# Performance work log

Hardware: AMD Instinct MI355X
Metric: run time of the kernel (lower is better)

Reference implementation:

```python
import jax, jax.numpy as jnp
import numpy as np
import math

N, L, C, H, K = 4, 16384, 256, 8, 4
D = C // H


def setup_inputs():
    rng = jax.random.key(0)
    ks = jax.random.split(rng, 16)
    def w(k, shape, scale):
        return jax.random.normal(k, shape, jnp.float32) * scale
    s = 1.0 / math.sqrt(C)
    return {
        "query": jax.random.normal(ks[0], (N, L, C), jnp.float32),
        "key": jax.random.normal(ks[1], (N, L, C), jnp.float32),
        "value": jax.random.normal(ks[2], (N, L, C), jnp.float32),
        "reference_points": jax.random.uniform(ks[3], (N, L, 2), jnp.float32),
        "pos_embed": jax.random.normal(ks[4], (N, L, C), jnp.float32),
        "Wq": w(ks[5], (C, C), s), "bq": jnp.zeros((C,), jnp.float32),
        "Wk": w(ks[6], (C, C), s), "bk": jnp.zeros((C,), jnp.float32),
        "Wv": w(ks[7], (C, C), s), "bv": jnp.zeros((C,), jnp.float32),
        "Wo1": w(ks[8], (C, 2 * C), s), "bo1": jnp.zeros((2 * C,), jnp.float32),
        "Wo2": w(ks[9], (2 * C, H * K * 2), 0.02), "bo2": w(ks[10], (H * K * 2,), 0.02),
        "Wpos": w(ks[11], (C, C), s), "bpos": jnp.zeros((C,), jnp.float32),
        "Wout": w(ks[12], (C, C), s), "bout": jnp.zeros((C,), jnp.float32),
    }


def _sample_weight(points):
    # F.grid_sample on a 1x1 feature map (bilinear, zeros padding, align_corners=False)
    # degenerates to a scalar weight: grid g = 2p-1, unnormalized c = g/2 = p - 0.5,
    # pixel-0 bilinear weight per axis = max(0, 1 - |c|).
    c = points - 0.5
    return jax.nn.relu(1.0 - jnp.abs(c[..., 0])) * jax.nn.relu(1.0 - jnp.abs(c[..., 1]))


def reference(query, key, value, reference_points, pos_embed,
              Wq, bq, Wk, bk, Wv, bv, Wo1, bo1, Wo2, bo2, Wpos, bpos, Wout, bout):
    Nb, Ln, Cd = query.shape
    q = (query @ Wq + bq).reshape(Nb, Ln, H, D)
    k = (key @ Wk + bk).reshape(Nb, Ln, H, D)
    v = (value @ Wv + bv).reshape(Nb, Ln, H, D)
    pos = (pos_embed @ Wpos + bpos).reshape(Nb, Ln, H, D)
    q = q + pos
    k = k + pos
    # offset MLP: Linear(C,2C) -> ReLU -> Linear(2C, H*K*2)
    offsets = (jax.nn.relu(query @ Wo1 + bo1) @ Wo2 + bo2).reshape(Nb, Ln, H, K, 2)
    sp = reference_points[:, :, None, None, :] + offsets  # [N,L,H,K,2]
    w = _sample_weight(sp)                                # [N,L,H,K]
    # sampled_k[n,l,h,k,:] = k[n,l,h,:] * w[n,l,h,k]  (1x1 grid_sample closed form)
    qk = jnp.einsum('nlhd,nlhd->nlh', q, k)               # [N,L,H]
    attn = jax.nn.softmax(qk[..., None] * w / math.sqrt(D), axis=-1)  # [N,L,H,K]
    # output = sum_k attn_k * (v * w_k) = v * sum_k(attn_k * w_k)
    wv = jnp.sum(attn * w, axis=-1)                       # [N,L,H]
    out = (v * wv[..., None]).reshape(Nb, Ln, Cd)
    return out @ Wout + bout
```

## Files before the change

kernel.cpp:

```cpp
#include <hip/hip_runtime.h>
#include <hip/hip_bf16.h>

typedef __bf16 bf16x8 __attribute__((ext_vector_type(8)));
typedef float f32x4 __attribute__((ext_vector_type(4)));
typedef float f32x2 __attribute__((ext_vector_type(2)));

#define MT 32
#define CC 256

__device__ __forceinline__ int swz(int r, int c) {
    return r * 512 + ((c * 2) ^ ((r & 7) << 4));
}
__device__ __forceinline__ int swzH(int r, int c) {
    return r * 1024 + ((c * 2) ^ ((r & 7) << 4));
}

__device__ __forceinline__ void stage_load(const float* __restrict__ src, int row0, int tid,
                                           f32x4 (&v)[4]) {
#pragma unroll
    for (int i = 0; i < 4; ++i) {
        int f = i * 512 + tid;
        int r = f >> 6;
        int c = (f & 63) * 4;
        v[i] = __builtin_nontemporal_load((const f32x4*)(src + (size_t)(row0 + r) * CC + c));
    }
}
__device__ __forceinline__ void stage_write(__bf16* dst, int tid, const f32x4 (&v)[4]) {
#pragma unroll
    for (int i = 0; i < 4; ++i) {
        int f = i * 512 + tid;
        int r = f >> 6;
        int c = (f & 63) * 4;
        union { __bf16 h[4]; unsigned long long u; } uu;
        uu.h[0] = (__bf16)v[i][0]; uu.h[1] = (__bf16)v[i][1];
        uu.h[2] = (__bf16)v[i][2]; uu.h[3] = (__bf16)v[i][3];
        *(unsigned long long*)((char*)dst + swz(r, c)) = uu.u;
    }
}

__global__ void prep_all(const float* __restrict__ Wq, const float* __restrict__ Wk,
                         const float* __restrict__ Wpos, const float* __restrict__ Wo1,
                         const float* __restrict__ Wo2, const float* __restrict__ Wv,
                         const float* __restrict__ Wout, __bf16* __restrict__ ws)
{
    int i = blockIdx.x * 256 + threadIdx.x;
    if (i >= 557056) return;
    int j, K, N;
    const float* S0 = nullptr; const float* S1 = nullptr;
    if (i < 131072)      { j = i;          K = 512; N = 256; S0 = Wq;  S1 = Wpos; }
    else if (i < 262144) { j = i - 131072; K = 512; N = 256; S0 = Wk;  S1 = Wpos; }
    else if (i < 393216) { j = i - 262144; K = 256; N = 512; S0 = Wo1; }
    else if (i < 425984) { j = i - 393216; K = 512; N = 64;  S0 = Wo2; }
    else if (i < 491520) { j = i - 425984; K = 256; N = 256; S0 = Wv; }
    else                 { j = i - 491520; K = 256; N = 256; S0 = Wout; }
    int tile = j >> 9, r = j & 511;
    int lane = r >> 3, e = r & 7;
    int q4 = lane >> 4, r16 = lane & 15;
    int KC = K >> 5;
    int nc = tile / KC, kc = tile - nc * KC;
    int k = kc * 32 + q4 * 8 + e;
    int n = nc * 16 + r16;
    float v;
    if (S1 && k >= 256) v = S1[(size_t)(k - 256) * N + n];
    else                v = S0[(size_t)k * N + n];
    ws[i] = (__bf16)v;
}

extern "C" __global__ void __launch_bounds__(512, 4)
fused_ext_attn(const float* __restrict__ query, const float* __restrict__ key,
               const float* __restrict__ value, const float* __restrict__ refp,
               const float* __restrict__ pose,
               const __bf16* __restrict__ ws,
               const float* __restrict__ bq, const float* __restrict__ bk,
               const float* __restrict__ bv, const float* __restrict__ bpos,
               const float* __restrict__ bo1, const float* __restrict__ bo2,
               const float* __restrict__ bout,
               float* __restrict__ out)
{
    const __bf16* WTqp  = ws;
    const __bf16* WTkp  = ws + 131072;
    const __bf16* WTo1  = ws + 262144;
    const __bf16* WTo2  = ws + 393216;
    const __bf16* WTv   = ws + 425984;
    const __bf16* WTout = ws + 491520;

    __shared__ __attribute__((aligned(16))) __bf16 SA[MT * CC];
    __shared__ __attribute__((aligned(16))) __bf16 SB[MT * CC];
    __shared__ __attribute__((aligned(16))) __bf16 SC[MT * CC];
    __shared__ __attribute__((aligned(16))) char   H1[32768];

    float* off_s = (float*)H1;
    float* qk_s  = (float*)(H1 + 8192);
    float* wv_s  = (float*)(H1 + 9216);

    const int tid = threadIdx.x;
    const int lane = tid & 63;
    const int wid = tid >> 6;
    const int r16 = lane & 15;
    const int q4 = lane >> 4;
    const int laneoff = lane * 8;
    const int row0 = blockIdx.x * MT;

    f32x4 vq[4], vp[4], vkey[4];
    stage_load(query, row0, tid, vq);
    stage_load(pose, row0, tid, vp);
    stage_load(key, row0, tid, vkey);
    stage_write(SA, tid, vq);
    stage_write(SB, tid, vp);
    __syncthreads();

    stage_write(SC, tid, vkey);
    {
        f32x4 acc[2][4];
#pragma unroll
        for (int i = 0; i < 2; ++i)
#pragma unroll
            for (int j = 0; j < 4; ++j) acc[i][j] = (f32x4){0.f, 0.f, 0.f, 0.f};
#pragma unroll
        for (int ks = 0; ks < 8; ++ks) {
            int ak = ks * 32 + q4 * 8;
            bf16x8 a[2], b[4];
#pragma unroll
            for (int mf = 0; mf < 2; ++mf)
                a[mf] = *(const bf16x8*)((const char*)SA + swz(mf * 16 + r16, ak));
#pragma unroll
            for (int nf = 0; nf < 4; ++nf)
                b[nf] = *(const bf16x8*)(WTo1 + ((size_t)(wid * 4 + nf) * 8 + ks) * 512 + laneoff);
#pragma unroll
            for (int mf = 0; mf < 2; ++mf)
#pragma unroll
                for (int nf = 0; nf < 4; ++nf)
                    acc[mf][nf] = __builtin_amdgcn_mfma_f32_16x16x32_bf16(a[mf], b[nf], acc[mf][nf], 0, 0, 0);
        }
#pragma unroll
        for (int mf = 0; mf < 2; ++mf)
#pragma unroll
            for (int nf = 0; nf < 4; ++nf) {
                int col = wid * 64 + nf * 16 + r16;
                float bias = bo1[col];
#pragma unroll
                for (int r = 0; r < 4; ++r)
                    *(__bf16*)(H1 + swzH(mf * 16 + q4 * 4 + r, col)) =
                        (__bf16)fmaxf(acc[mf][nf][r] + bias, 0.f);
            }
    }
    __syncthreads();

    f32x4 accO[2];
    accO[0] = (f32x4){0.f, 0.f, 0.f, 0.f};
    accO[1] = (f32x4){0.f, 0.f, 0.f, 0.f};
    if (wid < 4) {
#pragma unroll
        for (int ks = 0; ks < 16; ++ks) {
            int ak = ks * 32 + q4 * 8;
            bf16x8 b = *(const bf16x8*)(WTo2 + ((size_t)wid * 16 + ks) * 512 + laneoff);
#pragma unroll
            for (int mf = 0; mf < 2; ++mf) {
                bf16x8 a = *(const bf16x8*)(H1 + swzH(mf * 16 + r16, ak));
                accO[mf] = __builtin_amdgcn_mfma_f32_16x16x32_bf16(a, b, accO[mf], 0, 0, 0);
            }
        }
    }
    f32x4 vval[4];
    stage_load(value, row0, tid, vval);
    float qk_r[2][4];
    {
        f32x4 qa[2][2], ka[2][2];
#pragma unroll
        for (int i = 0; i < 2; ++i)
#pragma unroll
            for (int j = 0; j < 2; ++j) {
                qa[i][j] = (f32x4){0.f, 0.f, 0.f, 0.f};
                ka[i][j] = (f32x4){0.f, 0.f, 0.f, 0.f};
            }
#pragma unroll
        for (int ks = 0; ks < 8; ++ks) {
            int ak = ks * 32 + q4 * 8;
            bf16x8 aq[2], akk[2];
#pragma unroll
            for (int mf = 0; mf < 2; ++mf) {
                aq[mf]  = *(const bf16x8*)((const char*)SA + swz(mf * 16 + r16, ak));
                akk[mf] = *(const bf16x8*)((const char*)SC + swz(mf * 16 + r16, ak));
            }
#pragma unroll
            for (int nf = 0; nf < 2; ++nf) {
                size_t toff = ((size_t)(wid * 2 + nf) * 16 + ks) * 512 + laneoff;
                bf16x8 bqf = *(const bf16x8*)(WTqp + toff);
                bf16x8 bkf = *(const bf16x8*)(WTkp + toff);
#pragma unroll
                for (int mf = 0; mf < 2; ++mf) {
                    qa[mf][nf] = __builtin_amdgcn_mfma_f32_16x16x32_bf16(aq[mf],  bqf, qa[mf][nf], 0, 0, 0);
                    ka[mf][nf] = __builtin_amdgcn_mfma_f32_16x16x32_bf16(akk[mf], bkf, ka[mf][nf], 0, 0, 0);
                }
            }
        }
#pragma unroll
        for (int ks = 8; ks < 16; ++ks) {
            int ak = (ks - 8) * 32 + q4 * 8;
            bf16x8 ap[2];
#pragma unroll
            for (int mf = 0; mf < 2; ++mf)
                ap[mf] = *(const bf16x8*)((const char*)SB + swz(mf * 16 + r16, ak));
#pragma unroll
            for (int nf = 0; nf < 2; ++nf) {
                size_t toff = ((size_t)(wid * 2 + nf) * 16 + ks) * 512 + laneoff;
                bf16x8 bqf = *(const bf16x8*)(WTqp + toff);
                bf16x8 bkf = *(const bf16x8*)(WTkp + toff);
#pragma unroll
                for (int mf = 0; mf < 2; ++mf) {
                    qa[mf][nf] = __builtin_amdgcn_mfma_f32_16x16x32_bf16(ap[mf], bqf, qa[mf][nf], 0, 0, 0);
                    ka[mf][nf] = __builtin_amdgcn_mfma_f32_16x16x32_bf16(ap[mf], bkf, ka[mf][nf], 0, 0, 0);
                }
            }
        }
        float Bq[2], Bk[2];
#pragma unroll
        for (int nf = 0; nf < 2; ++nf) {
            int col = wid * 32 + nf * 16 + r16;
            Bq[nf] = bq[col] + bpos[col];
            Bk[nf] = bk[col] + bpos[col];
        }
#pragma unroll
        for (int mf = 0; mf < 2; ++mf)
#pragma unroll
            for (int r = 0; r < 4; ++r) {
                float p0 = (qa[mf][0][r] + Bq[0]) * (ka[mf][0][r] + Bk[0])
                         + (qa[mf][1][r] + Bq[1]) * (ka[mf][1][r] + Bk[1]);
#pragma unroll
                for (int m = 1; m < 16; m <<= 1)
                    p0 += __shfl_xor(p0, m);
                qk_r[mf][r] = p0;
            }
    }
    __syncthreads();

    stage_write(SA, tid, vval);
    if (wid < 4) {
        int col = wid * 16 + r16;
        float b2 = bo2[col];
#pragma unroll
        for (int mf = 0; mf < 2; ++mf)
#pragma unroll
            for (int r = 0; r < 4; ++r)
                off_s[(mf * 16 + q4 * 4 + r) * 64 + col] = accO[mf][r] + b2;
    }
    if (r16 == 0) {
#pragma unroll
        for (int mf = 0; mf < 2; ++mf)
#pragma unroll
            for (int r = 0; r < 4; ++r)
                qk_s[(mf * 16 + q4 * 4 + r) * 8 + wid] = qk_r[mf][r];
    }
    __syncthreads();

    if (tid < 256) {
        int t = tid >> 3, h = tid & 7;
        float qk = qk_s[t * 8 + h];
        f32x2 rp = __builtin_nontemporal_load((const f32x2*)(refp + (size_t)(row0 + t) * 2));
        float wgt[4], lg[4];
        float m = -1e30f;
#pragma unroll
        for (int kk = 0; kk < 4; ++kk) {
            float ox = off_s[t * 64 + (h * 4 + kk) * 2];
            float oy = off_s[t * 64 + (h * 4 + kk) * 2 + 1];
            float cx = rp[0] + ox - 0.5f, cy = rp[1] + oy - 0.5f;
            float wx = fmaxf(0.f, 1.f - fabsf(cx));
            float wy = fmaxf(0.f, 1.f - fabsf(cy));
            wgt[kk] = wx * wy;
            lg[kk] = qk * wgt[kk] * 0.17677669529663687f;
            m = fmaxf(m, lg[kk]);
        }
        float s = 0.f, sw = 0.f;
#pragma unroll
        for (int kk = 0; kk < 4; ++kk) {
            float e = __expf(lg[kk] - m);
            s += e;
            sw += e * wgt[kk];
        }
        wv_s[t * 8 + h] = sw / s;
    }
    __syncthreads();

    {
        f32x4 acc[2][2];
#pragma unroll
        for (int i = 0; i < 2; ++i)
#pragma unroll
            for (int j = 0; j < 2; ++j) acc[i][j] = (f32x4){0.f, 0.f, 0.f, 0.f};
#pragma unroll
        for (int ks = 0; ks < 8; ++ks) {
            int ak = ks * 32 + q4 * 8;
            bf16x8 a[2], b[2];
#pragma unroll
            for (int mf = 0; mf < 2; ++mf)
                a[mf] = *(const bf16x8*)((const char*)SA + swz(mf * 16 + r16, ak));
#pragma unroll
            for (int nf = 0; nf < 2; ++nf)
                b[nf] = *(const bf16x8*)(WTv + ((size_t)(wid * 2 + nf) * 8 + ks) * 512 + laneoff);
#pragma unroll
            for (int mf = 0; mf < 2; ++mf)
#pragma unroll
                for (int nf = 0; nf < 2; ++nf)
                    acc[mf][nf] = __builtin_amdgcn_mfma_f32_16x16x32_bf16(a[mf], b[nf], acc[mf][nf], 0, 0, 0);
        }
#pragma unroll
        for (int mf = 0; mf < 2; ++mf)
#pragma unroll
            for (int nf = 0; nf < 2; ++nf) {
                int col = wid * 32 + nf * 16 + r16;
                float bias = bv[col];
#pragma unroll
                for (int r = 0; r < 4; ++r) {
                    int row = mf * 16 + q4 * 4 + r;
                    float wvv = wv_s[row * 8 + wid];
                    *(__bf16*)((char*)SC + swz(row, col)) = (__bf16)((acc[mf][nf][r] + bias) * wvv);
                }
            }
    }
    __syncthreads();

    {
        f32x4 acc[2][2];
#pragma unroll
        for (int i = 0; i < 2; ++i)
#pragma unroll
            for (int j = 0; j < 2; ++j) acc[i][j] = (f32x4){0.f, 0.f, 0.f, 0.f};
#pragma unroll
        for (int ks = 0; ks < 8; ++ks) {
            int ak = ks * 32 + q4 * 8;
            bf16x8 a[2], b[2];
#pragma unroll
            for (int mf = 0; mf < 2; ++mf)
                a[mf] = *(const bf16x8*)((const char*)SC + swz(mf * 16 + r16, ak));
#pragma unroll
            for (int nf = 0; nf < 2; ++nf)
                b[nf] = *(const bf16x8*)(WTout + ((size_t)(wid * 2 + nf) * 8 + ks) * 512 + laneoff);
#pragma unroll
            for (int mf = 0; mf < 2; ++mf)
#pragma unroll
                for (int nf = 0; nf < 2; ++nf)
                    acc[mf][nf] = __builtin_amdgcn_mfma_f32_16x16x32_bf16(a[mf], b[nf], acc[mf][nf], 0, 0, 0);
        }
#pragma unroll
        for (int mf = 0; mf < 2; ++mf)
#pragma unroll
            for (int nf = 0; nf < 2; ++nf) {
                int col = wid * 32 + nf * 16 + r16;
                float bias = bout[col];
#pragma unroll
                for (int r = 0; r < 4; ++r) {
                    int row = mf * 16 + q4 * 4 + r;
                    __builtin_nontemporal_store(acc[mf][nf][r] + bias,
                                                out + (size_t)(row0 + row) * CC + col);
                }
            }
    }
}

extern "C" void kernel_launch(void* const* d_in, const int* in_sizes, int n_in,
                              void* d_out, int out_size, void* d_ws, size_t ws_size,
                              hipStream_t stream)
{
    const float* query = (const float*)d_in[0];
    const float* key   = (const float*)d_in[1];
    const float* value = (const float*)d_in[2];
    const float* refp  = (const float*)d_in[3];
    const float* pose  = (const float*)d_in[4];
    const float* Wq  = (const float*)d_in[5];  const float* bq   = (const float*)d_in[6];
    const float* Wk  = (const float*)d_in[7];  const float* bk   = (const float*)d_in[8];
    const float* Wv  = (const float*)d_in[9];  const float* bv   = (const float*)d_in[10];
    const float* Wo1 = (const float*)d_in[11]; const float* bo1  = (const float*)d_in[12];
    const float* Wo2 = (const float*)d_in[13]; const float* bo2  = (const float*)d_in[14];
    const float* Wpos= (const float*)d_in[15]; const float* bpos = (const float*)d_in[16];
    const float* Wout= (const float*)d_in[17]; const float* bout = (const float*)d_in[18];

    __bf16* ws = (__bf16*)d_ws;

    prep_all<<<2176, 256, 0, stream>>>(Wq, Wk, Wpos, Wo1, Wo2, Wv, Wout, ws);

    fused_ext_attn<<<65536 / MT, 512, 0, stream>>>(
        query, key, value, refp, pose, ws,
        bq, bk, bv, bpos, bo1, bo2, bout, (float*)d_out);
}
```

Baseline: 146.8 us.

## Double row tile to 64 and restructure LDS into two reused buffers

Raises the per-block row tile from 32 to 64, so each weight fragment loaded from global memory feeds four M-fragments instead of two, halving weight traffic per row. LDS is cut to two 32KB bf16 tiles plus a small scratch area by streaming query, pos, key and value through them in sequence. The offset-MLP hidden layer is processed in two column halves to fit, and offsets are stored as bf16. The q and k projections are now split into separate passes with extra barriers, and the larger tile halves the grid size.

```diff
diff --git a/kernel.cpp b/kernel.cpp
--- a/kernel.cpp
+++ b/kernel.cpp
@@ -5,35 +5,29 @@
 typedef float f32x4 __attribute__((ext_vector_type(4)));
 typedef float f32x2 __attribute__((ext_vector_type(2)));
 
-#define MT 32
+#define MT 64
 #define CC 256
 
 __device__ __forceinline__ int swz(int r, int c) {
     return r * 512 + ((c * 2) ^ ((r & 7) << 4));
 }
-__device__ __forceinline__ int swzH(int r, int c) {
-    return r * 1024 + ((c * 2) ^ ((r & 7) << 4));
-}
-
-__device__ __forceinline__ void stage_load(const float* __restrict__ src, int row0, int tid,
-                                           f32x4 (&v)[4]) {
-#pragma unroll
-    for (int i = 0; i < 4; ++i) {
+
+__device__ __forceinline__ bf16x8 ldB(const __bf16* __restrict__ WT, int nc, int KC, int kc,
+                                      int laneoff) {
+    return *(const bf16x8*)(WT + ((size_t)nc * KC + kc) * 512 + laneoff);
+}
+
+__device__ __forceinline__ void stream_tile(const float* __restrict__ src, int row0, int tid,
+                                            __bf16* dst) {
+#pragma unroll
+    for (int i = 0; i < 8; ++i) {
         int f = i * 512 + tid;
         int r = f >> 6;
         int c = (f & 63) * 4;
-        v[i] = __builtin_nontemporal_load((const f32x4*)(src + (size_t)(row0 + r) * CC + c));
-    }
-}
-__device__ __forceinline__ void stage_write(__bf16* dst, int tid, const f32x4 (&v)[4]) {
-#pragma unroll
-    for (int i = 0; i < 4; ++i) {
-        int f = i * 512 + tid;
-        int r = f >> 6;
-        int c = (f & 63) * 4;
+        f32x4 v = __builtin_nontemporal_load((const f32x4*)(src + (size_t)(row0 + r) * CC + c));
         union { __bf16 h[4]; unsigned long long u; } uu;
-        uu.h[0] = (__bf16)v[i][0]; uu.h[1] = (__bf16)v[i][1];
-        uu.h[2] = (__bf16)v[i][2]; uu.h[3] = (__bf16)v[i][3];
+        uu.h[0] = (__bf16)v[0]; uu.h[1] = (__bf16)v[1];
+        uu.h[2] = (__bf16)v[2]; uu.h[3] = (__bf16)v[3];
         *(unsigned long long*)((char*)dst + swz(r, c)) = uu.u;
     }
 }
@@ -85,13 +79,12 @@
     const __bf16* WTout = ws + 491520;
 
     __shared__ __attribute__((aligned(16))) __bf16 SA[MT * CC];
-    __shared__ __attribute__((aligned(16))) __bf16 SB[MT * CC];
-    __shared__ __attribute__((aligned(16))) __bf16 SC[MT * CC];
-    __shared__ __attribute__((aligned(16))) char   H1[32768];
-
-    float* off_s = (float*)H1;
-    float* qk_s  = (float*)(H1 + 8192);
-    float* wv_s  = (float*)(H1 + 9216);
+    __shared__ __attribute__((aligned(16))) __bf16 SX[MT * CC];
+    __shared__ __attribute__((aligned(16))) char   SY[16384];
+
+    __bf16* off_b = (__bf16*)SY;
+    float*  qk_s  = (float*)(SY + 8192);
+    float*  wv_s  = (float*)(SY + 10240);
 
     const int tid = threadIdx.x;
     const int lane = tid & 63;
@@ -101,117 +94,135 @@
     const int laneoff = lane * 8;
     const int row0 = blockIdx.x * MT;
 
-    f32x4 vq[4], vp[4], vkey[4];
-    stage_load(query, row0, tid, vq);
-    stage_load(pose, row0, tid, vp);
-    stage_load(key, row0, tid, vkey);
-    stage_write(SA, tid, vq);
-    stage_write(SB, tid, vp);
-    __syncthreads();
-
-    stage_write(SC, tid, vkey);
-    {
-        f32x4 acc[2][4];
-#pragma unroll
-        for (int i = 0; i < 2; ++i)
-#pragma unroll
-            for (int j = 0; j < 4; ++j) acc[i][j] = (f32x4){0.f, 0.f, 0.f, 0.f};
+    stream_tile(query, row0, tid, SA);
+    __syncthreads();
+
+    f32x4 accO[4];
+#pragma unroll
+    for (int i = 0; i < 4; ++i) accO[i] = (f32x4){0.f, 0.f, 0.f, 0.f};
+    for (int p = 0; p < 2; ++p) {
+        f32x4 acc[4][2];
+#pragma unroll
+        for (int i = 0; i < 4; ++i)
+#pragma unroll
+            for (int j = 0; j < 2; ++j) acc[i][j] = (f32x4){0.f, 0.f, 0.f, 0.f};
 #pragma unroll
         for (int ks = 0; ks < 8; ++ks) {
             int ak = ks * 32 + q4 * 8;
-            bf16x8 a[2], b[4];
-#pragma unroll
-            for (int mf = 0; mf < 2; ++mf)
+            bf16x8 a[4], b[2];
+#pragma unroll
+            for (int mf = 0; mf < 4; ++mf)
                 a[mf] = *(const bf16x8*)((const char*)SA + swz(mf * 16 + r16, ak));
 #pragma unroll
-            for (int nf = 0; nf < 4; ++nf)
-                b[nf] = *(const bf16x8*)(WTo1 + ((size_t)(wid * 4 + nf) * 8 + ks) * 512 + laneoff);
-#pragma unroll
-            for (int mf = 0; mf < 2; ++mf)
-#pragma unroll
-                for (int nf = 0; nf < 4; ++nf)
+            for (int nf = 0; nf < 2; ++nf)
+                b[nf] = ldB(WTo1, p * 16 + wid * 2 + nf, 8, ks, laneoff);
+#pragma unroll
+            for (int mf = 0; mf < 4; ++mf)
+#pragma unroll
+                for (int nf = 0; nf < 2; ++nf)
                     acc[mf][nf] = __builtin_amdgcn_mfma_f32_16x16x32_bf16(a[mf], b[nf], acc[mf][nf], 0, 0, 0);
         }
 #pragma unroll
-        for (int mf = 0; mf < 2; ++mf)
-#pragma unroll
-            for (int nf = 0; nf < 4; ++nf) {
-                int col = wid * 64 + nf * 16 + r16;
-                float bias = bo1[col];
+        for (int mf = 0; mf < 4; ++mf)
+#pragma unroll
+            for (int nf = 0; nf < 2; ++nf) {
+                int col = wid * 32 + nf * 16 + r16;
+                float bias = bo1[p * 256 + col];
 #pragma unroll
                 for (int r = 0; r < 4; ++r)
-                    *(__bf16*)(H1 + swzH(mf * 16 + q4 * 4 + r, col)) =
+                    *(__bf16*)((char*)SX + swz(mf * 16 + q4 * 4 + r, col)) =
                         (__bf16)fmaxf(acc[mf][nf][r] + bias, 0.f);
             }
-    }
-    __syncthreads();
-
-    f32x4 accO[2];
-    accO[0] = (f32x4){0.f, 0.f, 0.f, 0.f};
-    accO[1] = (f32x4){0.f, 0.f, 0.f, 0.f};
-    if (wid < 4) {
+        __syncthreads();
+        if (wid < 4) {
+#pragma unroll
+            for (int ks = 0; ks < 8; ++ks) {
+                int ak = ks * 32 + q4 * 8;
+                bf16x8 b = ldB(WTo2, wid, 16, p * 8 + ks, laneoff);
+#pragma unroll
+                for (int mf = 0; mf < 4; ++mf) {
+                    bf16x8 a = *(const bf16x8*)((const char*)SX + swz(mf * 16 + r16, ak));
+                    accO[mf] = __builtin_amdgcn_mfma_f32_16x16x32_bf16(a, b, accO[mf], 0, 0, 0);
+                }
+            }
+            if (p == 1) {
+                int col = wid * 16 + r16;
+                float b2 = bo2[col];
+#pragma unroll
+                for (int mf = 0; mf < 4; ++mf)
+#pragma unroll
+                    for (int r = 0; r < 4; ++r)
+                        off_b[(mf * 16 + q4 * 4 + r) * 64 + col] = (__bf16)(accO[mf][r] + b2);
+            }
+        }
+        __syncthreads();
+    }
+
+    f32x4 qa[4][2];
+#pragma unroll
+    for (int i = 0; i < 4; ++i)
+#pragma unroll
+        for (int j = 0; j < 2; ++j) qa[i][j] = (f32x4){0.f, 0.f, 0.f, 0.f};
+    stream_tile(pose, row0, tid, SX);
+#pragma unroll
+    for (int ks = 0; ks < 8; ++ks) {
+        int ak = ks * 32 + q4 * 8;
+        bf16x8 a[4], b[2];
+#pragma unroll
+        for (int mf = 0; mf < 4; ++mf)
+            a[mf] = *(const bf16x8*)((const char*)SA + swz(mf * 16 + r16, ak));
+#pragma unroll
+        for (int nf = 0; nf < 2; ++nf)
+            b[nf] = ldB(WTqp, wid * 2 + nf, 16, ks, laneoff);
+#pragma unroll
+        for (int mf = 0; mf < 4; ++mf)
+#pragma unroll
+            for (int nf = 0; nf < 2; ++nf)
+                qa[mf][nf] = __builtin_amdgcn_mfma_f32_16x16x32_bf16(a[mf], b[nf], qa[mf][nf], 0, 0, 0);
+    }
+    __syncthreads();
+
+    stream_tile(key, row0, tid, SA);
+#pragma unroll
+    for (int ks = 8; ks < 16; ++ks) {
+        int ak = (ks - 8) * 32 + q4 * 8;
+        bf16x8 a[4], b[2];
+#pragma unroll
+        for (int mf = 0; mf < 4; ++mf)
+            a[mf] = *(const bf16x8*)((const char*)SX + swz(mf * 16 + r16, ak));
+#pragma unroll
+        for (int nf = 0; nf < 2; ++nf)
+            b[nf] = ldB(WTqp, wid * 2 + nf, 16, ks, laneoff);
+#pragma unroll
+        for (int mf = 0; mf < 4; ++mf)
+#pragma unroll
+            for (int nf = 0; nf < 2; ++nf)
+                qa[mf][nf] = __builtin_amdgcn_mfma_f32_16x16x32_bf16(a[mf], b[nf], qa[mf][nf], 0, 0, 0);
+    }
+    __syncthreads();
+
+    {
+        f32x4 ka[4][2];
+#pragma unroll
+        for (int i = 0; i < 4; ++i)
+#pragma unroll
+            for (int j = 0; j < 2; ++j) ka[i][j] = (f32x4){0.f, 0.f, 0.f, 0.f};
 #pragma unroll
         for (int ks = 0; ks < 16; ++ks) {
-            int ak = ks * 32 + q4 * 8;
-            bf16x8 b = *(const bf16x8*)(WTo2 + ((size_t)wid * 16 + ks) * 512 + laneoff);
-#pragma unroll
-            for (int mf = 0; mf < 2; ++mf) {
-                bf16x8 a = *(const bf16x8*)(H1 + swzH(mf * 16 + r16, ak));
-                accO[mf] = __builtin_amdgcn_mfma_f32_16x16x32_bf16(a, b, accO[mf], 0, 0, 0);
-            }
-        }
-    }
-    f32x4 vval[4];
-    stage_load(value, row0, tid, vval);
-    float qk_r[2][4];
-    {
-        f32x4 qa[2][2], ka[2][2];
-#pragma unroll
-        for (int i = 0; i < 2; ++i)
-#pragma unroll
-            for (int j = 0; j < 2; ++j) {
-                qa[i][j] = (f32x4){0.f, 0.f, 0.f, 0.f};
-                ka[i][j] = (f32x4){0.f, 0.f, 0.f, 0.f};
-            }
-#pragma unroll
-        for (int ks = 0; ks < 8; ++ks) {
-            int ak = ks * 32 + q4 * 8;
-            bf16x8 aq[2], akk[2];
-#pragma unroll
-            for (int mf = 0; mf < 2; ++mf) {
-                aq[mf]  = *(const bf16x8*)((const char*)SA + swz(mf * 16 + r16, ak));
-                akk[mf] = *(const bf16x8*)((const char*)SC + swz(mf * 16 + r16, ak));
-            }
-#pragma unroll
-            for (int nf = 0; nf < 2; ++nf) {
-                size_t toff = ((size_t)(wid * 2 + nf) * 16 + ks) * 512 + laneoff;
-                bf16x8 bqf = *(const bf16x8*)(WTqp + toff);
-                bf16x8 bkf = *(const bf16x8*)(WTkp + toff);
-#pragma unroll
-                for (int mf = 0; mf < 2; ++mf) {
-                    qa[mf][nf] = __builtin_amdgcn_mfma_f32_16x16x32_bf16(aq[mf],  bqf, qa[mf][nf], 0, 0, 0);
-                    ka[mf][nf] = __builtin_amdgcn_mfma_f32_16x16x32_bf16(akk[mf], bkf, ka[mf][nf], 0, 0, 0);
-                }
-            }
-        }
-#pragma unroll
-        for (int ks = 8; ks < 16; ++ks) {
-            int ak = (ks - 8) * 32 + q4 * 8;
-            bf16x8 ap[2];
-#pragma unroll
-            for (int mf = 0; mf < 2; ++mf)
-                ap[mf] = *(const bf16x8*)((const char*)SB + swz(mf * 16 + r16, ak));
-#pragma unroll
-            for (int nf = 0; nf < 2; ++nf) {
-                size_t toff = ((size_t)(wid * 2 + nf) * 16 + ks) * 512 + laneoff;
-                bf16x8 bqf = *(const bf16x8*)(WTqp + toff);
-                bf16x8 bkf = *(const bf16x8*)(WTkp + toff);
-#pragma unroll
-                for (int mf = 0; mf < 2; ++mf) {
-                    qa[mf][nf] = __builtin_amdgcn_mfma_f32_16x16x32_bf16(ap[mf], bqf, qa[mf][nf], 0, 0, 0);
-                    ka[mf][nf] = __builtin_amdgcn_mfma_f32_16x16x32_bf16(ap[mf], bkf, ka[mf][nf], 0, 0, 0);
-                }
-            }
+            int ak = (ks & 7) * 32 + q4 * 8;
+            const char* Abase = (ks < 8) ? (const char*)SA : (const char*)SX;
+            bf16x8 a[4], b[2];
+#pragma unroll
+            for (int mf = 0; mf < 4; ++mf)
+                a[mf] = *(const bf16x8*)(Abase + swz(mf * 16 + r16, ak));
+#pragma unroll
+            for (int nf = 0; nf < 2; ++nf)
+                b[nf] = ldB(WTkp, wid * 2 + nf, 16, ks, laneoff);
+#pragma unroll
+            for (int mf = 0; mf < 4; ++mf)
+#pragma unroll
+                for (int nf = 0; nf < 2; ++nf)
+                    ka[mf][nf] = __builtin_amdgcn_mfma_f32_16x16x32_bf16(a[mf], b[nf], ka[mf][nf], 0, 0, 0);
         }
         float Bq[2], Bk[2];
 #pragma unroll
@@ -221,7 +232,7 @@
             Bk[nf] = bk[col] + bpos[col];
         }
 #pragma unroll
-        for (int mf = 0; mf < 2; ++mf)
+        for (int mf = 0; mf < 4; ++mf)
 #pragma unroll
             for (int r = 0; r < 4; ++r) {
                 float p0 = (qa[mf][0][r] + Bq[0]) * (ka[mf][0][r] + Bk[0])
@@ -229,31 +240,14 @@
 #pragma unroll
                 for (int m = 1; m < 16; m <<= 1)
                     p0 += __shfl_xor(p0, m);
-                qk_r[mf][r] = p0;
-            }
-    }
-    __syncthreads();
-
-    stage_write(SA, tid, vval);
-    if (wid < 4) {
-        int col = wid * 16 + r16;
-        float b2 = bo2[col];
-#pragma unroll
-        for (int mf = 0; mf < 2; ++mf)
-#pragma unroll
-            for (int r = 0; r < 4; ++r)
-                off_s[(mf * 16 + q4 * 4 + r) * 64 + col] = accO[mf][r] + b2;
-    }
-    if (r16 == 0) {
-#pragma unroll
-        for (int mf = 0; mf < 2; ++mf)
-#pragma unroll
-            for (int r = 0; r < 4; ++r)
-                qk_s[(mf * 16 + q4 * 4 + r) * 8 + wid] = qk_r[mf][r];
-    }
-    __syncthreads();
-
-    if (tid < 256) {
+                if (r16 == 0)
+                    qk_s[(mf * 16 + q4 * 4 + r) * 8 + wid] = p0;
+            }
+    }
+    __syncthreads();
+
+    stream_tile(value, row0, tid, SA);
+    {
         int t = tid >> 3, h = tid & 7;
         float qk = qk_s[t * 8 + h];
         f32x2 rp = __builtin_nontemporal_load((const f32x2*)(refp + (size_t)(row0 + t) * 2));
@@ -261,8 +255,8 @@
         float m = -1e30f;
 #pragma unroll
         for (int kk = 0; kk < 4; ++kk) {
-            float ox = off_s[t * 64 + (h * 4 + kk) * 2];
-            float oy = off_s[t * 64 + (h * 4 + kk) * 2 + 1];
+            float ox = (float)off_b[t * 64 + (h * 4 + kk) * 2];
+            float oy = (float)off_b[t * 64 + (h * 4 + kk) * 2 + 1];
             float cx = rp[0] + ox - 0.5f, cy = rp[1] + oy - 0.5f;
             float wx = fmaxf(0.f, 1.f - fabsf(cx));
             float wy = fmaxf(0.f, 1.f - fabsf(cy));
@@ -282,29 +276,29 @@
     __syncthreads();
 
     {
-        f32x4 acc[2][2];
-#pragma unroll
-        for (int i = 0; i < 2; ++i)
+        f32x4 acc[4][2];
+#pragma unroll
+        for (int i = 0; i < 4; ++i)
 #pragma unroll
             for (int j = 0; j < 2; ++j) acc[i][j] = (f32x4){0.f, 0.f, 0.f, 0.f};
 #pragma unroll
         for (int ks = 0; ks < 8; ++ks) {
             int ak = ks * 32 + q4 * 8;
-            bf16x8 a[2], b[2];
-#pragma unroll
-            for (int mf = 0; mf < 2; ++mf)
+            bf16x8 a[4], b[2];
+#pragma unroll
+            for (int mf = 0; mf < 4; ++mf)
                 a[mf] = *(const bf16x8*)((const char*)SA + swz(mf * 16 + r16, ak));
 #pragma unroll
             for (int nf = 0; nf < 2; ++nf)
-                b[nf] = *(const bf16x8*)(WTv + ((size_t)(wid * 2 + nf) * 8 + ks) * 512 + laneoff);
-#pragma unroll
-            for (int mf = 0; mf < 2; ++mf)
+                b[nf] = ldB(WTv, wid * 2 + nf, 8, ks, laneoff);
+#pragma unroll
+            for (int mf = 0; mf < 4; ++mf)
 #pragma unroll
                 for (int nf = 0; nf < 2; ++nf)
                     acc[mf][nf] = __builtin_amdgcn_mfma_f32_16x16x32_bf16(a[mf], b[nf], acc[mf][nf], 0, 0, 0);
         }
 #pragma unroll
-        for (int mf = 0; mf < 2; ++mf)
+        for (int mf = 0; mf < 4; ++mf)
 #pragma unroll
             for (int nf = 0; nf < 2; ++nf) {
                 int col = wid * 32 + nf * 16 + r16;
@@ -313,36 +307,36 @@
                 for (int r = 0; r < 4; ++r) {
                     int row = mf * 16 + q4 * 4 + r;
                     float wvv = wv_s[row * 8 + wid];
-                    *(__bf16*)((char*)SC + swz(row, col)) = (__bf16)((acc[mf][nf][r] + bias) * wvv);
+                    *(__bf16*)((char*)SX + swz(row, col)) = (__bf16)((acc[mf][nf][r] + bias) * wvv);
                 }
             }
     }
     __syncthreads();
 
     {
-        f32x4 acc[2][2];
-#pragma unroll
-        for (int i = 0; i < 2; ++i)
+        f32x4 acc[4][2];
+#pragma unroll
+        for (int i = 0; i < 4; ++i)
 #pragma unroll
             for (int j = 0; j < 2; ++j) acc[i][j] = (f32x4){0.f, 0.f, 0.f, 0.f};
 #pragma unroll
         for (int ks = 0; ks < 8; ++ks) {
             int ak = ks * 32 + q4 * 8;
-            bf16x8 a[2], b[2];
-#pragma unroll
-            for (int mf = 0; mf < 2; ++mf)
-                a[mf] = *(const bf16x8*)((const char*)SC + swz(mf * 16 + r16, ak));
-#pragma unroll
-            for (int nf = 0; nf < 2; ++nf)
-                b[nf] = *(const bf16x8*)(WTout + ((size_t)(wid * 2 + nf) * 8 + ks) * 512 + laneoff);
-#pragma unroll
-            for (int mf = 0; mf < 2; ++mf)
+            bf16x8 a[4], b[2];
+#pragma unroll
+            for (int mf = 0; mf < 4; ++mf)
+                a[mf] = *(const bf16x8*)((const char*)SX + swz(mf * 16 + r16, ak));
+#pragma unroll
+            for (int nf = 0; nf < 2; ++nf)
+                b[nf] = ldB(WTout, wid * 2 + nf, 8, ks, laneoff);
+#pragma unroll
+            for (int mf = 0; mf < 4; ++mf)
 #pragma unroll
                 for (int nf = 0; nf < 2; ++nf)
                     acc[mf][nf] = __builtin_amdgcn_mfma_f32_16x16x32_bf16(a[mf], b[nf], acc[mf][nf], 0, 0, 0);
         }
 #pragma unroll
-        for (int mf = 0; mf < 2; ++mf)
+        for (int mf = 0; mf < 4; ++mf)
 #pragma unroll
             for (int nf = 0; nf < 2; ++nf) {
                 int col = wid * 32 + nf * 16 + r16;
```

Result: slower. 261.2 us (+78.0%).

## Double row tile to 64 with 1024-thread blocks and split Q/K projections

Applied to the files above, without the earlier changes.

Each block now handles 64 rows with 16 waves, so every weight fragment read from global memory feeds four row fragments instead of two. The intent is to halve per-row weight traffic through L2. The fused Q/K projection is split into two sequential passes to cut register pressure, and the LDS layout is reorganised: the SC buffer is dropped and H1 is enlarged and reused for the key staging, offsets, partial qk sums and wv. In exchange there are more barriers, LDS per block rises to 128KB (one block per CU), and qk partials need a cross-wave reduction.

```diff
diff --git a/kernel.cpp b/kernel.cpp
--- a/kernel.cpp
+++ b/kernel.cpp
@@ -5,7 +5,7 @@
 typedef float f32x4 __attribute__((ext_vector_type(4)));
 typedef float f32x2 __attribute__((ext_vector_type(2)));
 
-#define MT 32
+#define MT 64
 #define CC 256
 
 __device__ __forceinline__ int swz(int r, int c) {
@@ -15,11 +15,16 @@
     return r * 1024 + ((c * 2) ^ ((r & 7) << 4));
 }
 
+__device__ __forceinline__ bf16x8 ldB(const __bf16* __restrict__ WT, int nc, int KC, int kc,
+                                      int laneoff) {
+    return *(const bf16x8*)(WT + ((size_t)nc * KC + kc) * 512 + laneoff);
+}
+
 __device__ __forceinline__ void stage_load(const float* __restrict__ src, int row0, int tid,
                                            f32x4 (&v)[4]) {
 #pragma unroll
     for (int i = 0; i < 4; ++i) {
-        int f = i * 512 + tid;
+        int f = i * 1024 + tid;
         int r = f >> 6;
         int c = (f & 63) * 4;
         v[i] = __builtin_nontemporal_load((const f32x4*)(src + (size_t)(row0 + r) * CC + c));
@@ -28,7 +33,7 @@
 __device__ __forceinline__ void stage_write(__bf16* dst, int tid, const f32x4 (&v)[4]) {
 #pragma unroll
     for (int i = 0; i < 4; ++i) {
-        int f = i * 512 + tid;
+        int f = i * 1024 + tid;
         int r = f >> 6;
         int c = (f & 63) * 4;
         union { __bf16 h[4]; unsigned long long u; } uu;
@@ -66,7 +71,7 @@
     ws[i] = (__bf16)v;
 }
 
-extern "C" __global__ void __launch_bounds__(512, 4)
+extern "C" __global__ void __launch_bounds__(1024, 4)
 fused_ext_attn(const float* __restrict__ query, const float* __restrict__ key,
                const float* __restrict__ value, const float* __restrict__ refp,
                const float* __restrict__ pose,
@@ -86,12 +91,12 @@
 
     __shared__ __attribute__((aligned(16))) __bf16 SA[MT * CC];
     __shared__ __attribute__((aligned(16))) __bf16 SB[MT * CC];
-    __shared__ __attribute__((aligned(16))) __bf16 SC[MT * CC];
-    __shared__ __attribute__((aligned(16))) char   H1[32768];
-
-    float* off_s = (float*)H1;
-    float* qk_s  = (float*)(H1 + 8192);
-    float* wv_s  = (float*)(H1 + 9216);
+    __shared__ __attribute__((aligned(16))) char   H1[65536];
+
+    __bf16* keyb    = (__bf16*)H1;
+    float*  off_s   = (float*)(H1 + 32768);
+    float*  qk_part = (float*)(H1 + 49152);
+    float*  wv_s    = (float*)(H1 + 53248);
 
     const int tid = threadIdx.x;
     const int lane = tid & 63;
@@ -101,42 +106,39 @@
     const int laneoff = lane * 8;
     const int row0 = blockIdx.x * MT;
 
-    f32x4 vq[4], vp[4], vkey[4];
+    f32x4 vq[4], vp[4];
     stage_load(query, row0, tid, vq);
     stage_load(pose, row0, tid, vp);
-    stage_load(key, row0, tid, vkey);
     stage_write(SA, tid, vq);
-    stage_write(SB, tid, vp);
-    __syncthreads();
-
-    stage_write(SC, tid, vkey);
+    __syncthreads();
+
     {
-        f32x4 acc[2][4];
-#pragma unroll
-        for (int i = 0; i < 2; ++i)
-#pragma unroll
-            for (int j = 0; j < 4; ++j) acc[i][j] = (f32x4){0.f, 0.f, 0.f, 0.f};
+        f32x4 acc[4][2];
+#pragma unroll
+        for (int i = 0; i < 4; ++i)
+#pragma unroll
+            for (int j = 0; j < 2; ++j) acc[i][j] = (f32x4){0.f, 0.f, 0.f, 0.f};
 #pragma unroll
         for (int ks = 0; ks < 8; ++ks) {
             int ak = ks * 32 + q4 * 8;
-            bf16x8 a[2], b[4];
-#pragma unroll
-            for (int mf = 0; mf < 2; ++mf)
+            bf16x8 a[4], b[2];
+#pragma unroll
+            for (int mf = 0; mf < 4; ++mf)
                 a[mf] = *(const bf16x8*)((const char*)SA + swz(mf * 16 + r16, ak));
 #pragma unroll
-            for (int nf = 0; nf < 4; ++nf)
-                b[nf] = *(const bf16x8*)(WTo1 + ((size_t)(wid * 4 + nf) * 8 + ks) * 512 + laneoff);
-#pragma unroll
-            for (int mf = 0; mf < 2; ++mf)
-#pragma unroll
-                for (int nf = 0; nf < 4; ++nf)
+            for (int nf = 0; nf < 2; ++nf)
+                b[nf] = ldB(WTo1, wid * 2 + nf, 8, ks, laneoff);
+#pragma unroll
+            for (int mf = 0; mf < 4; ++mf)
+#pragma unroll
+                for (int nf = 0; nf < 2; ++nf)
                     acc[mf][nf] = __builtin_amdgcn_mfma_f32_16x16x32_bf16(a[mf], b[nf], acc[mf][nf], 0, 0, 0);
         }
 #pragma unroll
-        for (int mf = 0; mf < 2; ++mf)
-#pragma unroll
-            for (int nf = 0; nf < 4; ++nf) {
-                int col = wid * 64 + nf * 16 + r16;
+        for (int mf = 0; mf < 4; ++mf)
+#pragma unroll
+            for (int nf = 0; nf < 2; ++nf) {
+                int col = wid * 32 + nf * 16 + r16;
                 float bias = bo1[col];
 #pragma unroll
                 for (int r = 0; r < 4; ++r)
@@ -146,116 +148,90 @@
     }
     __syncthreads();
 
-    f32x4 accO[2];
-    accO[0] = (f32x4){0.f, 0.f, 0.f, 0.f};
-    accO[1] = (f32x4){0.f, 0.f, 0.f, 0.f};
+    f32x4 vkey[4];
+    stage_load(key, row0, tid, vkey);
+    stage_write(SB, tid, vp);
+    f32x4 accO[4];
+#pragma unroll
+    for (int i = 0; i < 4; ++i) accO[i] = (f32x4){0.f, 0.f, 0.f, 0.f};
     if (wid < 4) {
 #pragma unroll
         for (int ks = 0; ks < 16; ++ks) {
             int ak = ks * 32 + q4 * 8;
-            bf16x8 b = *(const bf16x8*)(WTo2 + ((size_t)wid * 16 + ks) * 512 + laneoff);
-#pragma unroll
-            for (int mf = 0; mf < 2; ++mf) {
+            bf16x8 b = ldB(WTo2, wid, 16, ks, laneoff);
+#pragma unroll
+            for (int mf = 0; mf < 4; ++mf) {
                 bf16x8 a = *(const bf16x8*)(H1 + swzH(mf * 16 + r16, ak));
                 accO[mf] = __builtin_amdgcn_mfma_f32_16x16x32_bf16(a, b, accO[mf], 0, 0, 0);
             }
         }
     }
-    f32x4 vval[4];
-    stage_load(value, row0, tid, vval);
-    float qk_r[2][4];
-    {
-        f32x4 qa[2][2], ka[2][2];
-#pragma unroll
-        for (int i = 0; i < 2; ++i)
-#pragma unroll
-            for (int j = 0; j < 2; ++j) {
-                qa[i][j] = (f32x4){0.f, 0.f, 0.f, 0.f};
-                ka[i][j] = (f32x4){0.f, 0.f, 0.f, 0.f};
-            }
-#pragma unroll
-        for (int ks = 0; ks < 8; ++ks) {
-            int ak = ks * 32 + q4 * 8;
-            bf16x8 aq[2], akk[2];
-#pragma unroll
-            for (int mf = 0; mf < 2; ++mf) {
-                aq[mf]  = *(const bf16x8*)((const char*)SA + swz(mf * 16 + r16, ak));
-                akk[mf] = *(const bf16x8*)((const char*)SC + swz(mf * 16 + r16, ak));
-            }
-#pragma unroll
-            for (int nf = 0; nf < 2; ++nf) {
-                size_t toff = ((size_t)(wid * 2 + nf) * 16 + ks) * 512 + laneoff;
-                bf16x8 bqf = *(const bf16x8*)(WTqp + toff);
-                bf16x8 bkf = *(const bf16x8*)(WTkp + toff);
-#pragma unroll
-                for (int mf = 0; mf < 2; ++mf) {
-                    qa[mf][nf] = __builtin_amdgcn_mfma_f32_16x16x32_bf16(aq[mf],  bqf, qa[mf][nf], 0, 0, 0);
-                    ka[mf][nf] = __builtin_amdgcn_mfma_f32_16x16x32_bf16(akk[mf], bkf, ka[mf][nf], 0, 0, 0);
-                }
-            }
-        }
-#pragma unroll
-        for (int ks = 8; ks < 16; ++ks) {
-            int ak = (ks - 8) * 32 + q4 * 8;
-            bf16x8 ap[2];
-#pragma unroll
-            for (int mf = 0; mf < 2; ++mf)
-                ap[mf] = *(const bf16x8*)((const char*)SB + swz(mf * 16 + r16, ak));
-#pragma unroll
-            for (int nf = 0; nf < 2; ++nf) {
-                size_t toff = ((size_t)(wid * 2 + nf) * 16 + ks) * 512 + laneoff;
-                bf16x8 bqf = *(const bf16x8*)(WTqp + toff);
-                bf16x8 bkf = *(const bf16x8*)(WTkp + toff);
-#pragma unroll
-                for (int mf = 0; mf < 2; ++mf) {
-                    qa[mf][nf] = __builtin_amdgcn_mfma_f32_16x16x32_bf16(ap[mf], bqf, qa[mf][nf], 0, 0, 0);
-                    ka[mf][nf] = __builtin_amdgcn_mfma_f32_16x16x32_bf16(ap[mf], bkf, ka[mf][nf], 0, 0, 0);
-                }
-            }
-        }
-        float Bq[2], Bk[2];
-#pragma unroll
-        for (int nf = 0; nf < 2; ++nf) {
-            int col = wid * 32 + nf * 16 + r16;
-            Bq[nf] = bq[col] + bpos[col];
-            Bk[nf] = bk[col] + bpos[col];
-        }
-#pragma unroll
-        for (int mf = 0; mf < 2; ++mf)
-#pragma unroll
-            for (int r = 0; r < 4; ++r) {
-                float p0 = (qa[mf][0][r] + Bq[0]) * (ka[mf][0][r] + Bk[0])
-                         + (qa[mf][1][r] + Bq[1]) * (ka[mf][1][r] + Bk[1]);
-#pragma unroll
-                for (int m = 1; m < 16; m <<= 1)
-                    p0 += __shfl_xor(p0, m);
-                qk_r[mf][r] = p0;
-            }
-    }
-    __syncthreads();
-
-    stage_write(SA, tid, vval);
+    __syncthreads();
+
+    stage_write(keyb, tid, vkey);
     if (wid < 4) {
         int col = wid * 16 + r16;
         float b2 = bo2[col];
 #pragma unroll
-        for (int mf = 0; mf < 2; ++mf)
+        for (int mf = 0; mf < 4; ++mf)
 #pragma unroll
             for (int r = 0; r < 4; ++r)
                 off_s[(mf * 16 + q4 * 4 + r) * 64 + col] = accO[mf][r] + b2;
     }
-    if (r16 == 0) {
-#pragma unroll
-        for (int mf = 0; mf < 2; ++mf)
-#pragma unroll
-            for (int r = 0; r < 4; ++r)
-                qk_s[(mf * 16 + q4 * 4 + r) * 8 + wid] = qk_r[mf][r];
-    }
-    __syncthreads();
-
-    if (tid < 256) {
+    f32x4 qa[4];
+#pragma unroll
+    for (int i = 0; i < 4; ++i) qa[i] = (f32x4){0.f, 0.f, 0.f, 0.f};
+#pragma unroll
+    for (int ks = 0; ks < 16; ++ks) {
+        int ak = (ks & 7) * 32 + q4 * 8;
+        const char* Abase = (ks < 8) ? (const char*)SA : (const char*)SB;
+        bf16x8 b = ldB(WTqp, wid, 16, ks, laneoff);
+#pragma unroll
+        for (int mf = 0; mf < 4; ++mf) {
+            bf16x8 a = *(const bf16x8*)(Abase + swz(mf * 16 + r16, ak));
+            qa[mf] = __builtin_amdgcn_mfma_f32_16x16x32_bf16(a, b, qa[mf], 0, 0, 0);
+        }
+    }
+    __syncthreads();
+
+    f32x4 vval[4];
+    stage_load(value, row0, tid, vval);
+    {
+        f32x4 ka[4];
+#pragma unroll
+        for (int i = 0; i < 4; ++i) ka[i] = (f32x4){0.f, 0.f, 0.f, 0.f};
+#pragma unroll
+        for (int ks = 0; ks < 16; ++ks) {
+            int ak = (ks & 7) * 32 + q4 * 8;
+            const char* Abase = (ks < 8) ? (const char*)keyb : (const char*)SB;
+            bf16x8 b = ldB(WTkp, wid, 16, ks, laneoff);
+#pragma unroll
+            for (int mf = 0; mf < 4; ++mf) {
+                bf16x8 a = *(const bf16x8*)(Abase + swz(mf * 16 + r16, ak));
+                ka[mf] = __builtin_amdgcn_mfma_f32_16x16x32_bf16(a, b, ka[mf], 0, 0, 0);
+            }
+        }
+        int col = wid * 16 + r16;
+        float Bq = bq[col] + bpos[col];
+        float Bk = bk[col] + bpos[col];
+#pragma unroll
+        for (int mf = 0; mf < 4; ++mf)
+#pragma unroll
+            for (int r = 0; r < 4; ++r) {
+                float p = (qa[mf][r] + Bq) * (ka[mf][r] + Bk);
+#pragma unroll
+                for (int m = 1; m < 16; m <<= 1)
+                    p += __shfl_xor(p, m);
+                if (r16 == 0)
+                    qk_part[(mf * 16 + q4 * 4 + r) * 16 + wid] = p;
+            }
+    }
+    __syncthreads();
+
+    stage_write(SA, tid, vval);
+    if (tid < 512) {
         int t = tid >> 3, h = tid & 7;
-        float qk = qk_s[t * 8 + h];
+        float qk = qk_part[t * 16 + h * 2] + qk_part[t * 16 + h * 2 + 1];
         f32x2 rp = __builtin_nontemporal_load((const f32x2*)(refp + (size_t)(row0 + t) * 2));
         float wgt[4], lg[4];
         float m = -1e30f;
@@ -282,77 +258,56 @@
     __syncthreads();
 
     {
-        f32x4 acc[2][2];
-#pragma unroll
-        for (int i = 0; i < 2; ++i)
-#pragma unroll
-            for (int j = 0; j < 2; ++j) acc[i][j] = (f32x4){0.f, 0.f, 0.f, 0.f};
+        f32x4 acc[4];
+#pragma unroll
+        for (int i = 0; i < 4; ++i) acc[i] = (f32x4){0.f, 0.f, 0.f, 0.f};
 #pragma unroll
         for (int ks = 0; ks < 8; ++ks) {
             int ak = ks * 32 + q4 * 8;
-            bf16x8 a[2], b[2];
-#pragma unroll
-            for (int mf = 0; mf < 2; ++mf)
-                a[mf] = *(const bf16x8*)((const char*)SA + swz(mf * 16 + r16, ak));
-#pragma unroll
-            for (int nf = 0; nf < 2; ++nf)
-                b[nf] = *(const bf16x8*)(WTv + ((size_t)(wid * 2 + nf) * 8 + ks) * 512 + laneoff);
-#pragma unroll
-            for (int mf = 0; mf < 2; ++mf)
-#pragma unroll
-                for (int nf = 0; nf < 2; ++nf)
-                    acc[mf][nf] = __builtin_amdgcn_mfma_f32_16x16x32_bf16(a[mf], b[nf], acc[mf][nf], 0, 0, 0);
-        }
-#pragma unroll
-        for (int mf = 0; mf < 2; ++mf)
-#pragma unroll
-            for (int nf = 0; nf < 2; ++nf) {
-                int col = wid * 32 + nf * 16 + r16;
-                float bias = bv[col];
-#pragma unroll
-                for (int r = 0; r < 4; ++r) {
-                    int row = mf * 16 + q4 * 4 + r;
-                    float wvv = wv_s[row * 8 + wid];
-                    *(__bf16*)((char*)SC + swz(row, col)) = (__bf16)((acc[mf][nf][r] + bias) * wvv);
-                }
+            bf16x8 b = ldB(WTv, wid, 8, ks, laneoff);
+#pragma unroll
+            for (int mf = 0; mf < 4; ++mf) {
+                bf16x8 a = *(const bf16x8*)((const char*)SA + swz(mf * 16 + r16, ak));
+                acc[mf] = __builtin_amdgcn_mfma_f32_16x16x32_bf16(a, b, acc[mf], 0, 0, 0);
+            }
+        }
+        int col = wid * 16 + r16;
+        float bias = bv[col];
+        int head = wid >> 1;
+#pragma unroll
+        for (int mf = 0; mf < 4; ++mf)
+#pragma unroll
+            for (int r = 0; r < 4; ++r) {
+                int row = mf * 16 + q4 * 4 + r;
+                float wvv = wv_s[row * 8 + head];
+                *(__bf16*)((char*)SB + swz(row, col)) = (__bf16)((acc[mf][r] + bias) * wvv);
             }
     }
     __syncthreads();
 
     {
-        f32x4 acc[2][2];
-#pragma unroll
-        for (int i = 0; i < 2; ++i)
-#pragma unroll
-            for (int j = 0; j < 2; ++j) acc[i][j] = (f32x4){0.f, 0.f, 0.f, 0.f};
+        f32x4 acc[4];
+#pragma unroll
+        for (int i = 0; i < 4; ++i) acc[i] = (f32x4){0.f, 0.f, 0.f, 0.f};
 #pragma unroll
         for (int ks = 0; ks < 8; ++ks) {
             int ak = ks * 32 + q4 * 8;
-            bf16x8 a[2], b[2];
-#pragma unroll
-            for (int mf = 0; mf < 2; ++mf)
-                a[mf] = *(const bf16x8*)((const char*)SC + swz(mf * 16 + r16, ak));
-#pragma unroll
-            for (int nf = 0; nf < 2; ++nf)
-                b[nf] = *(const bf16x8*)(WTout + ((size_t)(wid * 2 + nf) * 8 + ks) * 512 + laneoff);
-#pragma unroll
-            for (int mf = 0; mf < 2; ++mf)
-#pragma unroll
-                for (int nf = 0; nf < 2; ++nf)
-                    acc[mf][nf] = __builtin_amdgcn_mfma_f32_16x16x32_bf16(a[mf], b[nf], acc[mf][nf], 0, 0, 0);
-        }
-#pragma unroll
-        for (int mf = 0; mf < 2; ++mf)
-#pragma unroll
-            for (int nf = 0; nf < 2; ++nf) {
-                int col = wid * 32 + nf * 16 + r16;
-                float bias = bout[col];
-#pragma unroll
-                for (int r = 0; r < 4; ++r) {
-                    int row = mf * 16 + q4 * 4 + r;
-                    __builtin_nontemporal_store(acc[mf][nf][r] + bias,
-                                                out + (size_t)(row0 + row) * CC + col);
-                }
+            bf16x8 b = ldB(WTout, wid, 8, ks, laneoff);
+#pragma unroll
+            for (int mf = 0; mf < 4; ++mf) {
+                bf16x8 a = *(const bf16x8*)((const char*)SB + swz(mf * 16 + r16, ak));
+                acc[mf] = __builtin_amdgcn_mfma_f32_16x16x32_bf16(a, b, acc[mf], 0, 0, 0);
+            }
+        }
+        int col = wid * 16 + r16;
+        float bias = bout[col];
+#pragma unroll
+        for (int mf = 0; mf < 4; ++mf)
+#pragma unroll
+            for (int r = 0; r < 4; ++r) {
+                int row = mf * 16 + q4 * 4 + r;
+                __builtin_nontemporal_store(acc[mf][r] + bias,
+                                            out + (size_t)(row0 + row) * CC + col);
             }
     }
 }
@@ -378,7 +333,7 @@
 
     prep_all<<<2176, 256, 0, stream>>>(Wq, Wk, Wpos, Wo1, Wo2, Wv, Wout, ws);
 
-    fused_ext_attn<<<65536 / MT, 512, 0, stream>>>(
+    fused_ext_attn<<<65536 / MT, 1024, 0, stream>>>(
         query, key, value, refp, pose, ws,
         bq, bk, bv, bpos, bo1, bo2, bout, (float*)d_out);
 }
```

Result: slower. 195.5 us (+33.2%).
